# Performance work log

Measured on AMD Instinct MI355X. Metric: run time of the kernel, lower is better.

## Reference

```python
import jax, jax.numpy as jnp
import numpy as np

B, T, U = 8, 200, 50
D_ENC, D_DEC, D_FUSION, VOCAB = 512, 512, 640, 1024


def setup_inputs() -> dict:
    key = jax.random.key(0)
    ks = jax.random.split(key, 11)
    s = lambda d: 1.0 / np.sqrt(d)
    return {
        "encoder_out": jax.random.normal(ks[0], (B, T, D_ENC), jnp.float32),
        "decoder_out": jax.random.normal(ks[1], (B, U, D_DEC), jnp.float32),
        "ot_decoder_feature": jax.random.normal(ks[2], (B, T, D_DEC), jnp.float32),
        "W_enc": jax.random.uniform(ks[3], (D_ENC, D_FUSION), jnp.float32, -s(D_ENC), s(D_ENC)),
        "b_enc": jax.random.uniform(ks[4], (D_FUSION,), jnp.float32, -s(D_ENC), s(D_ENC)),
        "W_ot": jax.random.uniform(ks[5], (D_DEC, D_FUSION), jnp.float32, -s(D_DEC), s(D_DEC)),
        "b_ot": jax.random.uniform(ks[6], (D_FUSION,), jnp.float32, -s(D_DEC), s(D_DEC)),
        "W_dec": jax.random.uniform(ks[7], (D_DEC, D_FUSION), jnp.float32, -s(D_DEC), s(D_DEC)),
        "b_dec": jax.random.uniform(ks[8], (D_FUSION,), jnp.float32, -s(D_DEC), s(D_DEC)),
        "W_out": jax.random.uniform(ks[9], (D_FUSION, VOCAB), jnp.float32, -s(D_FUSION), s(D_FUSION)),
        "b_out": jax.random.uniform(ks[10], (VOCAB,), jnp.float32, -s(D_FUSION), s(D_FUSION)),
    }


def reference(encoder_out, decoder_out, ot_decoder_feature,
              W_enc, b_enc, W_ot, b_ot, W_dec, b_dec, W_out, b_out):
    # proj_enc + proj_ot_dec: both [B, T, d_fusion]
    fused = (jnp.einsum('bte,ef->btf', encoder_out, W_enc) + b_enc
             + jnp.einsum('btd,df->btf', ot_decoder_feature, W_ot) + b_ot)
    proj_dec = jnp.einsum('bud,df->buf', decoder_out, W_dec) + b_dec  # [B, U, d_fusion]
    # broadcast add over T x U, tanh, then final projection to vocab
    joint = jnp.tanh(fused[:, :, None, :] + proj_dec[:, None, :, :])  # [B, T, U, d_fusion]
    logits = jnp.einsum('btuf,fv->btuv', joint, W_out) + b_out  # [B, T, U, vocab]
    return logits
```

## Files before the change

### kernel.cpp

```cpp
#include <hip/hip_runtime.h>
#include <math.h>

typedef __bf16 bf16_t;
typedef __bf16 bf16x8 __attribute__((ext_vector_type(8)));
typedef float f32x4 __attribute__((ext_vector_type(4)));
typedef int i32x4 __attribute__((ext_vector_type(4)));
typedef int i32x2 __attribute__((ext_vector_type(2)));

#define SW_SCALE 0.03952847075f

#define GLOAD_LDS16(g, l)                                                      \
  __builtin_amdgcn_global_load_lds(                                            \
      (const __attribute__((address_space(1))) void*)(g),                      \
      (__attribute__((address_space(3))) void*)(l), 16, 0, 0)

__global__ __launch_bounds__(256) void prep_kernel(
    const float* __restrict__ enc, const float* __restrict__ dec,
    const float* __restrict__ ot, const float* __restrict__ W_enc,
    const float* __restrict__ W_ot, const float* __restrict__ W_dec,
    const float* __restrict__ W_out, bf16_t* __restrict__ Acat,
    bf16_t* __restrict__ Dec, bf16_t* __restrict__ WcatT,
    bf16_t* __restrict__ WdecT, signed char* __restrict__ WoutT8) {
  __shared__ float T[32][33];
  const int tid = threadIdx.x;
  const int b = blockIdx.x;

  if (b < 900) {
    const int idx8 = (b * 256 + tid) * 8;
    const int N0 = 1600 * 1024;
    if (idx8 < N0) {
      const int r = idx8 >> 10, c = idx8 & 1023;
      const float* src = (c < 512) ? enc + (r << 9) + c : ot + (r << 9) + c - 512;
      f32x4 v0 = *(const f32x4*)src;
      f32x4 v1 = *(const f32x4*)(src + 4);
      bf16x8 o;
#pragma unroll
      for (int e = 0; e < 4; ++e) {
        o[e] = (bf16_t)v0[e];
        o[e + 4] = (bf16_t)v1[e];
      }
      *(bf16x8*)(Acat + idx8) = o;
    } else {
      const int j = idx8 - N0;
      if (j < 400 * 512) {
        f32x4 v0 = *(const f32x4*)(dec + j);
        f32x4 v1 = *(const f32x4*)(dec + j + 4);
        bf16x8 o;
#pragma unroll
        for (int e = 0; e < 4; ++e) {
          o[e] = (bf16_t)v0[e];
          o[e + 4] = (bf16_t)v1[e];
        }
        *(bf16x8*)(Dec + j) = o;
      }
    }
    return;
  }

  const int tx = tid & 31, ty = tid >> 5;
  if (b < 1540) {
    const int b2 = b - 900;
    const int kt = b2 / 20, ft = b2 - kt * 20;
    const int k0 = kt * 32, f0 = ft * 32;
#pragma unroll
    for (int j = 0; j < 4; ++j) {
      const int kk = k0 + ty + j * 8;
      T[ty + j * 8][tx] = (kk < 512) ? W_enc[kk * 640 + f0 + tx]
                                     : W_ot[(kk - 512) * 640 + f0 + tx];
    }
    __syncthreads();
#pragma unroll
    for (int j = 0; j < 4; ++j) {
      const int ff = f0 + ty + j * 8;
      WcatT[ff * 1024 + k0 + tx] = (bf16_t)T[tx][ty + j * 8];
    }
    return;
  }
  if (b < 1860) {
    const int b2 = b - 1540;
    const int kt = b2 / 20, ft = b2 - kt * 20;
    const int k0 = kt * 32, f0 = ft * 32;
#pragma unroll
    for (int j = 0; j < 4; ++j)
      T[ty + j * 8][tx] = W_dec[(k0 + ty + j * 8) * 640 + f0 + tx];
    __syncthreads();
#pragma unroll
    for (int j = 0; j < 4; ++j) {
      const int ff = f0 + ty + j * 8;
      WdecT[ff * 512 + k0 + tx] = (bf16_t)T[tx][ty + j * 8];
    }
    return;
  }
  {
    const int b2 = b - 1860;
    const int vt = b2 / 20, ft = b2 - vt * 20;
    const int v0 = vt * 32, f0 = ft * 32;
#pragma unroll
    for (int j = 0; j < 4; ++j)
      T[ty + j * 8][tx] = W_out[(f0 + ty + j * 8) * 1024 + v0 + tx];
    __syncthreads();
#pragma unroll
    for (int j = 0; j < 4; ++j) {
      const int vv = v0 + ty + j * 8;
      float w = T[tx][ty + j * 8] * (127.0f / SW_SCALE);
      w = fminf(fmaxf(w, -127.0f), 127.0f);
      WoutT8[(size_t)vv * 640 + f0 + tx] = (signed char)__float2int_rn(w);
    }
  }
}

__global__ __launch_bounds__(256) void stage1_kernel(
    const bf16_t* __restrict__ Acat, const bf16_t* __restrict__ WcatT,
    const float* __restrict__ b_enc, const float* __restrict__ b_ot,
    float* __restrict__ ta, const bf16_t* __restrict__ Dec,
    const bf16_t* __restrict__ WdecT, const float* __restrict__ b_dec,
    float* __restrict__ tb) {
  __shared__ __align__(16) unsigned char L[3][16384];
  const int tid = threadIdx.x;
  const int wid = tid >> 6, l = tid & 63;
  const int wm = wid >> 1, wn = wid & 1;

  const bool big = (blockIdx.y < 25);
  const int M = big ? 1600 : 400;
  const int K = big ? 1024 : 512;
  const bf16_t* A = big ? Acat : Dec;
  const bf16_t* Bt = big ? WcatT : WdecT;
  const float* bias1 = big ? b_enc : b_dec;
  const float* bias2 = big ? b_ot : nullptr;
  float* out = big ? ta : tb;
  const int r0 = (big ? blockIdx.y : blockIdx.y - 25) * 64;
  const int n0 = blockIdx.x * 64;

  const int sperm = ((l & 3) ^ ((l >> 3) & 3)) * 8;
  int ra0 = r0 + wm * 32 + (l >> 2);
  if (ra0 > M - 1) ra0 = M - 1;
  int ra1 = r0 + wm * 32 + 16 + (l >> 2);
  if (ra1 > M - 1) ra1 = M - 1;
  const bf16_t* gA0 = A + (size_t)ra0 * K + sperm;
  const bf16_t* gA1 = A + (size_t)ra1 * K + sperm;
  const bf16_t* gB0 = Bt + (size_t)(n0 + wn * 32 + (l >> 2)) * K + sperm;
  const bf16_t* gB1 = gB0 + (size_t)16 * K;
  const int wb = wid * 4096;

  const int lr = l & 15, kg = l >> 4;
  const int swz = (kg ^ ((lr >> 1) & 3)) << 4;
  const int aO = wb + lr * 64 + swz;
  const int bO = wb + 2048 + lr * 64 + swz;

#define ST1_STAGE(t, s)                                                        \
  {                                                                            \
    GLOAD_LDS16(gA0 + (t) * 32, L[s] + wb);                                    \
    GLOAD_LDS16(gA1 + (t) * 32, L[s] + wb + 1024);                             \
    GLOAD_LDS16(gB0 + (t) * 32, L[s] + wb + 2048);                             \
    GLOAD_LDS16(gB1 + (t) * 32, L[s] + wb + 3072);                             \
  }

  f32x4 acc[2][2] = {};
  const int steps = K >> 5;
  ST1_STAGE(0, 0);
  ST1_STAGE(1, 1);
#pragma unroll 1
  for (int ks = 0; ks < steps; ++ks) {
    const int cur = ks % 3;
    if (ks < steps - 2) {
      ST1_STAGE(ks + 2, (ks + 2) % 3);
      __builtin_amdgcn_sched_barrier(0);
      asm volatile("s_waitcnt vmcnt(8)" ::: "memory");
    } else if (ks == steps - 2) {
      asm volatile("s_waitcnt vmcnt(4)" ::: "memory");
    } else {
      asm volatile("s_waitcnt vmcnt(0)" ::: "memory");
    }
    __builtin_amdgcn_sched_barrier(0);
    bf16x8 af[2], bfr[2];
#pragma unroll
    for (int a = 0; a < 2; ++a)
      af[a] = *(const bf16x8*)(L[cur] + aO + a * 1024);
#pragma unroll
    for (int b = 0; b < 2; ++b)
      bfr[b] = *(const bf16x8*)(L[cur] + bO + b * 1024);
#pragma unroll
    for (int a = 0; a < 2; ++a)
#pragma unroll
      for (int b = 0; b < 2; ++b)
        acc[a][b] = __builtin_amdgcn_mfma_f32_16x16x32_bf16(af[a], bfr[b],
                                                            acc[a][b], 0, 0, 0);
  }
#undef ST1_STAGE

#pragma unroll
  for (int a = 0; a < 2; ++a)
#pragma unroll
    for (int b = 0; b < 2; ++b) {
      int col = n0 + wn * 32 + b * 16 + lr;
      float bv = bias1[col] + (bias2 ? bias2[col] : 0.0f);
#pragma unroll
      for (int j = 0; j < 4; ++j) {
        int rg = r0 + wm * 32 + a * 16 + kg * 4 + j;
        if (rg < M) out[(size_t)rg * 640 + col] = tanhf(acc[a][b][j] + bv);
      }
    }
}

__global__ __launch_bounds__(256) void materialize8_kernel(
    const float* __restrict__ ta,
    const float* __restrict__ tb,
    signed char* __restrict__ A8) {
  const int idx = blockIdx.x * 256 + threadIdx.x;
  const int row = idx / 80;
  const int c8 = idx - row * 80;
  const int frow = row / 50;
  const int bidx = row / 10000;
  const int u = row - frow * 50;
  const float* tap = ta + (size_t)frow * 640 + c8 * 8;
  const float* tbp = tb + (size_t)(bidx * 50 + u) * 640 + c8 * 8;
  f32x4 xa0 = *(const f32x4*)tap, xa1 = *(const f32x4*)(tap + 4);
  f32x4 xb0 = *(const f32x4*)tbp, xb1 = *(const f32x4*)(tbp + 4);
  int q[8];
#pragma unroll
  for (int e = 0; e < 4; ++e) {
    float d0 = fmaxf(1.0f + xa0[e] * xb0[e], 1e-6f);
    q[e] = __float2int_rn((xa0[e] + xb0[e]) * __builtin_amdgcn_rcpf(d0) * 127.0f);
    float d1 = fmaxf(1.0f + xa1[e] * xb1[e], 1e-6f);
    q[e + 4] =
        __float2int_rn((xa1[e] + xb1[e]) * __builtin_amdgcn_rcpf(d1) * 127.0f);
  }
  i32x2 pk;
  pk[0] = (q[0] & 255) | ((q[1] & 255) << 8) | ((q[2] & 255) << 16) | (q[3] << 24);
  pk[1] = (q[4] & 255) | ((q[5] & 255) << 8) | ((q[6] & 255) << 16) | (q[7] << 24);
  *(i32x2*)(A8 + (size_t)row * 656 + c8 * 8) = pk;
}

__global__ __launch_bounds__(512, 6) void joint_gemm_kernel(
    const signed char* __restrict__ A8,
    const signed char* __restrict__ W8,
    const float* __restrict__ b_out,
    float* __restrict__ out) {
  __shared__ __align__(16) signed char Al[2][21504];
  __shared__ __align__(16) float Tr[8][16 * 20];
  const int tid = threadIdx.x;
  const int w = tid >> 6, l = tid & 63;
  const int lr = l & 15, kg = l >> 4;

  const int orig = blockIdx.x;
  const int mg = (orig & 7) + 8 * (orig >> 6);
  const int strip = (orig >> 3) & 7;
  if (mg >= 313) return;
  const int c0w = strip * 128 + w * 16;

  i32x4 Bf[10];
  const signed char* gW = W8 + (size_t)(c0w + lr) * 640 + kg * 16;
#pragma unroll
  for (int t = 0; t < 10; ++t) Bf[t] = *(const i32x4*)(gW + t * 64);
  const float bv = b_out[c0w + lr];

  const int i0 = w * 3;
  const int ni = (i0 < 21) ? ((i0 + 3 <= 21) ? 3 : 21 - i0) : 0;
  const size_t mbase = (size_t)mg * 256 * 656;

#define JSTAGE(c, buf)                                                         \
  {                                                                            \
    const signed char* s_ = A8 + mbase + (size_t)(c) * (32 * 656);             \
    for (int k_ = 0; k_ < ni; ++k_) {                                          \
      const int i_ = i0 + k_;                                                  \
      const int off_ = (i_ == 20) ? 19968 : i_ * 1024;                         \
      GLOAD_LDS16(s_ + off_ + l * 16, Al[buf] + off_);                         \
    }                                                                          \
  }

  JSTAGE(0, 0);

  const float cfac = SW_SCALE / (127.0f * 127.0f);
  float* trw = Tr[w];
  const int part = l & 3;
  const int srow = l >> 2;

#pragma unroll 1
  for (int c = 0; c < 8; ++c) {
    const int buf = c & 1;
    if (c < 7) JSTAGE(c + 1, buf ^ 1);
    __builtin_amdgcn_sched_barrier(0);
    if (c == 0) {
      asm volatile("s_waitcnt vmcnt(3)" ::: "memory");
    } else if (c < 7) {
      asm volatile("s_waitcnt vmcnt(7)" ::: "memory");
    } else {
      asm volatile("s_waitcnt vmcnt(4)" ::: "memory");
    }
    __builtin_amdgcn_sched_barrier(0);
    __builtin_amdgcn_s_barrier();
    __builtin_amdgcn_sched_barrier(0);

    i32x4 acc0 = {}, acc1 = {};
#pragma unroll
    for (int t = 0; t < 10; ++t) {
      i32x4 a0 = *(const i32x4*)(Al[buf] + lr * 656 + t * 64 + kg * 16);
      i32x4 a1 = *(const i32x4*)(Al[buf] + (16 + lr) * 656 + t * 64 + kg * 16);
      acc0 = __builtin_amdgcn_mfma_i32_16x16x64_i8(a0, Bf[t], acc0, 0, 0, 0);
      acc1 = __builtin_amdgcn_mfma_i32_16x16x64_i8(a1, Bf[t], acc1, 0, 0, 0);
    }

#pragma unroll
    for (int j = 0; j < 4; ++j)
      trw[(kg * 4 + j) * 20 + lr] = (float)acc0[j] * cfac + bv;
    asm volatile("s_waitcnt lgkmcnt(0)" ::: "memory");
    {
      f32x4 v = *(const f32x4*)(trw + srow * 20 + part * 4);
      asm volatile("s_waitcnt lgkmcnt(0)" ::: "memory");
      const int grow = mg * 256 + c * 32 + srow;
      if (grow < 80000)
        __builtin_nontemporal_store(
            v, (f32x4*)(out + (size_t)grow * 1024 + c0w + part * 4));
    }
#pragma unroll
    for (int j = 0; j < 4; ++j)
      trw[(kg * 4 + j) * 20 + lr] = (float)acc1[j] * cfac + bv;
    asm volatile("s_waitcnt lgkmcnt(0)" ::: "memory");
    {
      f32x4 v = *(const f32x4*)(trw + srow * 20 + part * 4);
      asm volatile("s_waitcnt lgkmcnt(0)" ::: "memory");
      const int grow = mg * 256 + c * 32 + 16 + srow;
      if (grow < 80000)
        __builtin_nontemporal_store(
            v, (f32x4*)(out + (size_t)grow * 1024 + c0w + part * 4));
    }
    __builtin_amdgcn_sched_barrier(0);
    __builtin_amdgcn_s_barrier();
  }
#undef JSTAGE
}

extern "C" void kernel_launch(void* const* d_in, const int* in_sizes, int n_in,
                              void* d_out, int out_size, void* d_ws,
                              size_t ws_size, hipStream_t stream) {
  const float* enc = (const float*)d_in[0];
  const float* dec = (const float*)d_in[1];
  const float* ot = (const float*)d_in[2];
  const float* W_enc = (const float*)d_in[3];
  const float* b_enc = (const float*)d_in[4];
  const float* W_ot = (const float*)d_in[5];
  const float* b_ot = (const float*)d_in[6];
  const float* W_dec = (const float*)d_in[7];
  const float* b_dec = (const float*)d_in[8];
  const float* W_out = (const float*)d_in[9];
  const float* b_out = (const float*)d_in[10];
  float* out = (float*)d_out;

  char* ws = (char*)d_ws;
  size_t off = 0;
  auto alloc = [&](size_t bytes) {
    void* p = ws + off;
    off += (bytes + 255) & ~(size_t)255;
    return p;
  };
  float* ta = (float*)alloc(1600 * 640 * 4);
  float* tb = (float*)alloc(400 * 640 * 4);
  bf16_t* Acat = (bf16_t*)alloc(1600 * 1024 * 2);
  bf16_t* Dec = (bf16_t*)alloc(400 * 512 * 2);
  bf16_t* WcatT = (bf16_t*)alloc(640 * 1024 * 2);
  bf16_t* WdecT = (bf16_t*)alloc(640 * 512 * 2);
  signed char* WoutT8 = (signed char*)alloc(1024 * 640);
  signed char* A8 = (signed char*)alloc((size_t)80128 * 656);

  prep_kernel<<<2500, 256, 0, stream>>>(enc, dec, ot, W_enc, W_ot, W_dec,
                                        W_out, Acat, Dec, WcatT, WdecT, WoutT8);
  stage1_kernel<<<dim3(10, 32), 256, 0, stream>>>(Acat, WcatT, b_enc, b_ot, ta,
                                                  Dec, WdecT, b_dec, tb);
  materialize8_kernel<<<25000, 256, 0, stream>>>(ta, tb, A8);
  joint_gemm_kernel<<<2560, 512, 0, stream>>>(A8, WoutT8, b_out, out);
}
```

Baseline: 132.3 us.

## Fuse int8 joint-activation generation into the joint GEMM kernel

Drops the separate materialize kernel and its int8 A8 buffer. Each GEMM block now computes the quantized tanh-sum rows straight from ta/tb, writes them into LDS, and double-buffers the next chunk after the current MFMAs. This removes the global write and re-read of the large int8 activation matrix and one kernel launch. In exchange, each of the eight column strips recomputes the same activation rows, and the fp32 ta/tb loads are only partly hidden behind the GEMM work.

```diff
diff --git a/kernel.cpp b/kernel.cpp
--- a/kernel.cpp
+++ b/kernel.cpp
@@ -202,37 +202,9 @@
     }
 }
 
-__global__ __launch_bounds__(256) void materialize8_kernel(
+__global__ __launch_bounds__(512, 6) void joint_gemm_kernel(
     const float* __restrict__ ta,
     const float* __restrict__ tb,
-    signed char* __restrict__ A8) {
-  const int idx = blockIdx.x * 256 + threadIdx.x;
-  const int row = idx / 80;
-  const int c8 = idx - row * 80;
-  const int frow = row / 50;
-  const int bidx = row / 10000;
-  const int u = row - frow * 50;
-  const float* tap = ta + (size_t)frow * 640 + c8 * 8;
-  const float* tbp = tb + (size_t)(bidx * 50 + u) * 640 + c8 * 8;
-  f32x4 xa0 = *(const f32x4*)tap, xa1 = *(const f32x4*)(tap + 4);
-  f32x4 xb0 = *(const f32x4*)tbp, xb1 = *(const f32x4*)(tbp + 4);
-  int q[8];
-#pragma unroll
-  for (int e = 0; e < 4; ++e) {
-    float d0 = fmaxf(1.0f + xa0[e] * xb0[e], 1e-6f);
-    q[e] = __float2int_rn((xa0[e] + xb0[e]) * __builtin_amdgcn_rcpf(d0) * 127.0f);
-    float d1 = fmaxf(1.0f + xa1[e] * xb1[e], 1e-6f);
-    q[e + 4] =
-        __float2int_rn((xa1[e] + xb1[e]) * __builtin_amdgcn_rcpf(d1) * 127.0f);
-  }
-  i32x2 pk;
-  pk[0] = (q[0] & 255) | ((q[1] & 255) << 8) | ((q[2] & 255) << 16) | (q[3] << 24);
-  pk[1] = (q[4] & 255) | ((q[5] & 255) << 8) | ((q[6] & 255) << 16) | (q[7] << 24);
-  *(i32x2*)(A8 + (size_t)row * 656 + c8 * 8) = pk;
-}
-
-__global__ __launch_bounds__(512, 6) void joint_gemm_kernel(
-    const signed char* __restrict__ A8,
     const signed char* __restrict__ W8,
     const float* __restrict__ b_out,
     float* __restrict__ out) {
@@ -254,21 +226,48 @@
   for (int t = 0; t < 10; ++t) Bf[t] = *(const i32x4*)(gW + t * 64);
   const float bv = b_out[c0w + lr];
 
-  const int i0 = w * 3;
-  const int ni = (i0 < 21) ? ((i0 + 3 <= 21) ? 3 : 21 - i0) : 0;
-  const size_t mbase = (size_t)mg * 256 * 656;
-
-#define JSTAGE(c, buf)                                                         \
+  int rowq[5], c8q[5];
+#pragma unroll
+  for (int q = 0; q < 5; ++q) {
+    const int g = tid + q * 512;
+    rowq[q] = g / 80;
+    c8q[q] = g - rowq[q] * 80;
+  }
+
+#define JGEN(cc, dst)                                                          \
   {                                                                            \
-    const signed char* s_ = A8 + mbase + (size_t)(c) * (32 * 656);             \
-    for (int k_ = 0; k_ < ni; ++k_) {                                          \
-      const int i_ = i0 + k_;                                                  \
-      const int off_ = (i_ == 20) ? 19968 : i_ * 1024;                         \
-      GLOAD_LDS16(s_ + off_ + l * 16, Al[buf] + off_);                         \
+    const int rb_ = mg * 256 + (cc) * 32;                                      \
+    _Pragma("unroll") for (int q = 0; q < 5; ++q) {                            \
+      int r_ = rb_ + rowq[q];                                                  \
+      if (r_ > 79999) r_ = 79999;             \
+      const int fr_ = r_ / 50;                                                 \
+      const int u_ = r_ - fr_ * 50;                                            \
+      const int bi_ = r_ / 10000;                                              \
+      const float* tap_ = ta + (size_t)fr_ * 640 + c8q[q] * 8;                 \
+      const float* tbp_ = tb + (size_t)(bi_ * 50 + u_) * 640 + c8q[q] * 8;     \
+      f32x4 xa0_ = *(const f32x4*)tap_, xa1_ = *(const f32x4*)(tap_ + 4);      \
+      f32x4 xb0_ = *(const f32x4*)tbp_, xb1_ = *(const f32x4*)(tbp_ + 4);      \
+      int qv_[8];                                                              \
+      _Pragma("unroll") for (int e = 0; e < 4; ++e) {                          \
+        float d0_ = fmaxf(1.0f + xa0_[e] * xb0_[e], 1e-6f);                    \
+        qv_[e] = __float2int_rn((xa0_[e] + xb0_[e]) *                          \
+                                __builtin_amdgcn_rcpf(d0_) * 127.0f);          \
+        float d1_ = fmaxf(1.0f + xa1_[e] * xb1_[e], 1e-6f);                    \
+        qv_[e + 4] = __float2int_rn((xa1_[e] + xb1_[e]) *                      \
+                                    __builtin_amdgcn_rcpf(d1_) * 127.0f);      \
+      }                                                                        \
+      i32x2 pk_;                                                               \
+      pk_[0] = (qv_[0] & 255) | ((qv_[1] & 255) << 8) |                        \
+               ((qv_[2] & 255) << 16) | (qv_[3] << 24);                        \
+      pk_[1] = (qv_[4] & 255) | ((qv_[5] & 255) << 8) |                        \
+               ((qv_[6] & 255) << 16) | (qv_[7] << 24);                        \
+      *(i32x2*)((dst) + rowq[q] * 656 + c8q[q] * 8) = pk_;                     \
     }                                                                          \
   }
 
-  JSTAGE(0, 0);
+  JGEN(0, Al[0]);
+  asm volatile("s_waitcnt lgkmcnt(0)" ::: "memory");
+  __builtin_amdgcn_s_barrier();
 
   const float cfac = SW_SCALE / (127.0f * 127.0f);
   float* trw = Tr[w];
@@ -278,19 +277,6 @@
 #pragma unroll 1
   for (int c = 0; c < 8; ++c) {
     const int buf = c & 1;
-    if (c < 7) JSTAGE(c + 1, buf ^ 1);
-    __builtin_amdgcn_sched_barrier(0);
-    if (c == 0) {
-      asm volatile("s_waitcnt vmcnt(3)" ::: "memory");
-    } else if (c < 7) {
-      asm volatile("s_waitcnt vmcnt(7)" ::: "memory");
-    } else {
-      asm volatile("s_waitcnt vmcnt(4)" ::: "memory");
-    }
-    __builtin_amdgcn_sched_barrier(0);
-    __builtin_amdgcn_s_barrier();
-    __builtin_amdgcn_sched_barrier(0);
-
     i32x4 acc0 = {}, acc1 = {};
 #pragma unroll
     for (int t = 0; t < 10; ++t) {
@@ -299,6 +285,9 @@
       acc0 = __builtin_amdgcn_mfma_i32_16x16x64_i8(a0, Bf[t], acc0, 0, 0, 0);
       acc1 = __builtin_amdgcn_mfma_i32_16x16x64_i8(a1, Bf[t], acc1, 0, 0, 0);
     }
+    __builtin_amdgcn_sched_barrier(0);
+    if (c < 7) JGEN(c + 1, Al[buf ^ 1]);
+    __builtin_amdgcn_sched_barrier(0);
 
 #pragma unroll
     for (int j = 0; j < 4; ++j)
@@ -327,7 +316,7 @@
     __builtin_amdgcn_sched_barrier(0);
     __builtin_amdgcn_s_barrier();
   }
-#undef JSTAGE
+#undef JGEN
 }
 
 extern "C" void kernel_launch(void* const* d_in, const int* in_sizes, int n_in,
@@ -360,12 +349,10 @@
   bf16_t* WcatT = (bf16_t*)alloc(640 * 1024 * 2);
   bf16_t* WdecT = (bf16_t*)alloc(640 * 512 * 2);
   signed char* WoutT8 = (signed char*)alloc(1024 * 640);
-  signed char* A8 = (signed char*)alloc((size_t)80128 * 656);
 
   prep_kernel<<<2500, 256, 0, stream>>>(enc, dec, ot, W_enc, W_ot, W_dec,
                                         W_out, Acat, Dec, WcatT, WdecT, WoutT8);
   stage1_kernel<<<dim3(10, 32), 256, 0, stream>>>(Acat, WcatT, b_enc, b_ot, ta,
                                                   Dec, WdecT, b_dec, tb);
-  materialize8_kernel<<<25000, 256, 0, stream>>>(ta, tb, A8);
-  joint_gemm_kernel<<<2560, 512, 0, stream>>>(A8, WoutT8, b_out, out);
+  joint_gemm_kernel<<<2560, 512, 0, stream>>>(ta, tb, WoutT8, b_out, out);
 }
```

Measured after the change: 343.3 us. 159% more time.
